# Performance work log

Hardware: AMD Instinct MI355X
Metric: run time of the kernel (lower is better)

## Reference

```python
import jax, jax.numpy as jnp
import numpy as np

D_MODEL = 2048
NUM_HEADS = 16
D_FF = 8192
EPS = 1e-5


def setup_inputs() -> dict:
    key = jax.random.key(0)
    ks = jax.random.split(key, 9)
    s = 0.02
    return {
        "x": jax.random.normal(ks[0], (2, 2048, D_MODEL), dtype=jnp.float32),
        "wq": jax.random.normal(ks[1], (D_MODEL, D_MODEL), dtype=jnp.float32) * s,
        "wk": jax.random.normal(ks[2], (D_MODEL, D_MODEL), dtype=jnp.float32) * s,
        "wv": jax.random.normal(ks[3], (D_MODEL, D_MODEL), dtype=jnp.float32) * s,
        "wo": jax.random.normal(ks[4], (D_MODEL, D_MODEL), dtype=jnp.float32) * s,
        "w1": jax.random.normal(ks[5], (D_FF, D_MODEL), dtype=jnp.float32) * s,
        "w2": jax.random.normal(ks[6], (D_MODEL, D_FF), dtype=jnp.float32) * s,
        "g1": jnp.ones((D_MODEL,), dtype=jnp.float32),
        "g2": jnp.ones((D_MODEL,), dtype=jnp.float32),
    }


def rmsnorm(a, g):
    rms = jnp.sqrt(jnp.sum(a * a, axis=-1, keepdims=True) / a.shape[-1] + EPS)
    return a / rms * g


def attention(xn, wq, wk, wv, wo):
    B, S, D = xn.shape
    H, dk = NUM_HEADS, D // NUM_HEADS
    # Linear weights are (out, in); y = x @ W^T
    q = (xn @ wq.T).reshape(B, S, H, dk).transpose(0, 2, 1, 3)  # bhsd
    k = (xn @ wk.T).reshape(B, S, H, dk).transpose(0, 2, 1, 3)
    v = (xn @ wv.T).reshape(B, S, H, dk).transpose(0, 2, 1, 3)
    scores = jnp.einsum("bhqd,bhkd->bhqk", q, k) * (dk ** -0.5)
    causal = jnp.triu(jnp.ones((S, S), dtype=bool), k=1)
    scores = jnp.where(causal, -jnp.inf, scores)
    probs = jax.nn.softmax(scores, axis=-1)
    out = jnp.einsum("bhqk,bhkd->bhqd", probs, v)
    out = out.transpose(0, 2, 1, 3).reshape(B, S, D)
    return out @ wo.T


def reference(x, wq, wk, wv, wo, w1, w2, g1, g2):
    x = x + attention(rmsnorm(x, g1), wq, wk, wv, wo)
    h = jax.nn.gelu(rmsnorm(x, g2) @ w1.T, approximate=False)
    x = x + h @ w2.T
    return x
```

## Files before the change

### kernel.cpp

```cpp
#include <hip/hip_runtime.h>
#include <hip/hip_bf16.h>
#include <math.h>

#define D_MODEL 2048
#define SEQ     2048
#define BATCH   2
#define NHEAD   16
#define DK      128
#define DFF     8192
#define MROWS   (BATCH*SEQ)

typedef short short8 __attribute__((ext_vector_type(8)));
typedef float f32x4  __attribute__((ext_vector_type(4)));

__device__ __forceinline__ short f2bf(float f) {
  union { __hip_bfloat16 b; short s; } u;
  u.b = __float2bfloat16(f);
  return u.s;
}

__device__ __forceinline__ void gload_lds16(const void* g, void* l) {
  __builtin_amdgcn_global_load_lds(
      (const __attribute__((address_space(1))) unsigned int*)g,
      (__attribute__((address_space(3))) unsigned int*)l, 16, 0, 0);
}

__global__ __launch_bounds__(256) void rmsnorm_k(const float* __restrict__ x,
                                                 const float* __restrict__ g,
                                                 short* __restrict__ o) {
  const int row = blockIdx.x;
  const int t = threadIdx.x;
  const float4* xr = (const float4*)(x + (size_t)row * D_MODEL);
  const float4* gr = (const float4*)g;
  float4 v0 = xr[2*t], v1 = xr[2*t+1];
  float s = v0.x*v0.x + v0.y*v0.y + v0.z*v0.z + v0.w*v0.w
          + v1.x*v1.x + v1.y*v1.y + v1.z*v1.z + v1.w*v1.w;
  #pragma unroll
  for (int off = 1; off < 64; off <<= 1) s += __shfl_xor(s, off);
  __shared__ float red[4];
  if ((t & 63) == 0) red[t >> 6] = s;
  __syncthreads();
  float tot = red[0] + red[1] + red[2] + red[3];
  float inv = rsqrtf(tot * (1.0f / D_MODEL) + 1e-5f);
  float4 g0 = gr[2*t], g1v = gr[2*t+1];
  short8 ov;
  ov[0] = f2bf(v0.x * inv * g0.x);
  ov[1] = f2bf(v0.y * inv * g0.y);
  ov[2] = f2bf(v0.z * inv * g0.z);
  ov[3] = f2bf(v0.w * inv * g0.w);
  ov[4] = f2bf(v1.x * inv * g1v.x);
  ov[5] = f2bf(v1.y * inv * g1v.y);
  ov[6] = f2bf(v1.z * inv * g1v.z);
  ov[7] = f2bf(v1.w * inv * g1v.w);
  *((short8*)(o + (size_t)row * D_MODEL) + t) = ov;
}

__global__ __launch_bounds__(256) void f2b_k(const float* __restrict__ src,
                                             short* __restrict__ dst, int n8) {
  int i = blockIdx.x * 256 + threadIdx.x;
  if (i >= n8) return;
  const float4* s4 = (const float4*)src + 2 * (size_t)i;
  float4 a = s4[0], b = s4[1];
  short8 o = { f2bf(a.x), f2bf(a.y), f2bf(a.z), f2bf(a.w),
               f2bf(b.x), f2bf(b.y), f2bf(b.z), f2bf(b.w) };
  *((short8*)dst + i) = o;
}

template<int EPI>
__global__ __launch_bounds__(256) void gemm_fast(const short* __restrict__ A,
                                                 const short* __restrict__ B,
                                                 void* Cv,
                                                 const float* __restrict__ resid,
                                                 int M, int N, int K) {
  __shared__ __align__(16) short As[128 * 64];
  __shared__ __align__(16) short Bs[128 * 64];
  const int t = threadIdx.x;
  const int m0 = blockIdx.x * 128, n0 = blockIdx.y * 128;
  const int wave = t >> 6, lane = t & 63, lr = lane & 15, lg = lane >> 4;
  const int wr = (wave >> 1) * 64, wc = (wave & 1) * 64;

  f32x4 acc[4][4];
  const f32x4 z4 = {0.f, 0.f, 0.f, 0.f};
  #pragma unroll
  for (int m = 0; m < 4; ++m)
    #pragma unroll
    for (int n = 0; n < 4; ++n) acc[m][n] = z4;

  const int srow = t >> 3;
  const int scol = (t & 7) * 8;

  for (int k0 = 0; k0 < K; k0 += 64) {
    #pragma unroll
    for (int i = 0; i < 4; ++i) {
      int r = srow + 32 * i;
      gload_lds16(A + (size_t)(m0 + r) * K + k0 + scol, &As[r * 64 + scol]);
      gload_lds16(B + (size_t)(n0 + r) * K + k0 + scol, &Bs[r * 64 + scol]);
    }
    __syncthreads();
    #pragma unroll
    for (int kk = 0; kk < 64; kk += 32) {
      short8 af[4], bfr[4];
      #pragma unroll
      for (int m = 0; m < 4; ++m) af[m]  = *(const short8*)&As[(wr + m*16 + lr) * 64 + kk + lg*8];
      #pragma unroll
      for (int n = 0; n < 4; ++n) bfr[n] = *(const short8*)&Bs[(wc + n*16 + lr) * 64 + kk + lg*8];
      #pragma unroll
      for (int m = 0; m < 4; ++m)
        #pragma unroll
        for (int n = 0; n < 4; ++n)
          acc[m][n] = __builtin_amdgcn_mfma_f32_16x16x32_bf16(af[m], bfr[n], acc[m][n], 0, 0, 0);
    }
    __syncthreads();
  }

  #pragma unroll
  for (int m = 0; m < 4; ++m)
    #pragma unroll
    for (int n = 0; n < 4; ++n)
      #pragma unroll
      for (int r = 0; r < 4; ++r) {
        int row = m0 + wr + m*16 + lg*4 + r;
        int col = n0 + wc + n*16 + lr;
        size_t idx = (size_t)row * N + col;
        float vv = acc[m][n][r];
        if (EPI == 0) {
          ((short*)Cv)[idx] = f2bf(vv);
        } else if (EPI == 1) {
          float gl = 0.5f * vv * (1.0f + erff(vv * 0.70710678118654752f));
          ((short*)Cv)[idx] = f2bf(gl);
        } else {
          ((float*)Cv)[idx] = vv + resid[idx];
        }
      }
}

__global__ __launch_bounds__(256) void vtrans(const short* __restrict__ QKV,
                                              short* __restrict__ VT) {
  const int st = blockIdx.x;
  const int bh = blockIdx.y;
  const int b = bh >> 4, h = bh & 15;
  const int t = threadIdx.x;
  __shared__ __align__(16) short T[64 * 128];
  const short* Vsrc = QKV + ((size_t)b * SEQ) * 6144 + 2 * D_MODEL + h * DK;
  {
    int r = t >> 4, c = (t & 15) * 8;
    #pragma unroll
    for (int i = 0; i < 4; ++i) {
      int rr = r + 16 * i;
      uint4 vv = *(const uint4*)(Vsrc + (size_t)(st * 64 + rr) * 6144 + c);
      *(uint4*)&T[rr * 128 + (c ^ (((rr >> 3) & 7) << 3))] = vv;
    }
  }
  __syncthreads();
  short* dst = VT + ((size_t)bh * DK) * SEQ + st * 64;
  {
    int c2 = (t & 7) * 8;
    #pragma unroll
    for (int i = 0; i < 4; ++i) {
      int d = (t >> 3) + 32 * i;
      short8 ov;
      #pragma unroll
      for (int j = 0; j < 8; ++j)
        ov[j] = T[(c2 + j) * 128 + (d ^ ((((c2 + j) >> 3) & 7) << 3))];
      *(short8*)(dst + (size_t)d * SEQ + c2) = ov;
    }
  }
}

__global__ __launch_bounds__(512, 2) void attn3(const short* __restrict__ QKV,
                                                const short* __restrict__ VT,
                                                short* __restrict__ O) {
  const float SC = 0.12751743f;
  const int a = blockIdx.x, bh = blockIdx.y;
  const int b = bh >> 4, h = bh & 15;
  const int t = threadIdx.x, w = t >> 6, lane = t & 63, lr = lane & 15, lg = lane >> 4;
  const short* Qp = QKV + ((size_t)b * SEQ) * 6144 + h * DK;
  const short* Kp = Qp + D_MODEL;
  const short* Vp = VT + ((size_t)bh * DK) * SEQ;
  __shared__ __align__(16) short Ks[2][64 * 128];
  __shared__ __align__(16) short Vs[2][128 * 64];
  __shared__ __align__(16) short Ps[8][16][72];

  const int krr = t >> 4, kcc = (t & 15) * 8;
  const int vdd = t >> 3, vcc = (t & 7) * 8;
  const f32x4 z4 = {0.f, 0.f, 0.f, 0.f};

  for (int sub = 0; sub < 2; ++sub) {
    const int ts = sub ? (15 - a) : a;
    const int nt = 2 * ts + 2;
    const int qrow0 = ts * 128 + w * 16;

    short8 qf[4];
    #pragma unroll
    for (int ki = 0; ki < 4; ++ki)
      qf[ki] = *(const short8*)(Qp + (size_t)(qrow0 + lr) * 6144 + ki * 32 + lg * 8);

    f32x4 acc[8];
    #pragma unroll
    for (int nd = 0; nd < 8; ++nd) acc[nd] = z4;
    float mrow[4], lsum[4];
    #pragma unroll
    for (int r = 0; r < 4; ++r) { mrow[r] = -INFINITY; lsum[r] = 0.f; }

    uint4 krg[2], vrg[2];
    #pragma unroll
    for (int i = 0; i < 2; ++i) {
      krg[i] = *(const uint4*)(Kp + (size_t)(krr + 32 * i) * 6144 + kcc);
      vrg[i] = *(const uint4*)(Vp + (size_t)(vdd + 64 * i) * SEQ + vcc);
    }
    __syncthreads();
    #pragma unroll
    for (int i = 0; i < 2; ++i) {
      int r = krr + 32 * i;
      *(uint4*)&Ks[0][(r * 128 + kcc) ^ ((r & 7) << 3)] = krg[i];
      int d = vdd + 64 * i;
      *(uint4*)&Vs[0][(d * 64 + vcc) ^ ((d & 7) << 3)] = vrg[i];
    }
    __syncthreads();

    int cur = 0;
    for (int tt = 0; tt < nt; ++tt) {
      const bool pre = (tt + 1 < nt);
      if (pre) {
        #pragma unroll
        for (int i = 0; i < 2; ++i) {
          krg[i] = *(const uint4*)(Kp + (size_t)((tt + 1) * 64 + krr + 32 * i) * 6144 + kcc);
          vrg[i] = *(const uint4*)(Vp + (size_t)(vdd + 64 * i) * SEQ + (tt + 1) * 64 + vcc);
        }
      }

      f32x4 sf[4] = {z4, z4, z4, z4};
      #pragma unroll
      for (int ki = 0; ki < 4; ++ki) {
        #pragma unroll
        for (int nk = 0; nk < 4; ++nk) {
          int rr = nk * 16 + lr;
          short8 kf = *(const short8*)&Ks[cur][(rr * 128 + ki * 32 + lg * 8) ^ ((rr & 7) << 3)];
          sf[nk] = __builtin_amdgcn_mfma_f32_16x16x32_bf16(qf[ki], kf, sf[nk], 0, 0, 0);
        }
      }

      const bool diag = (tt * 64 + 63 > qrow0);
      #pragma unroll
      for (int r = 0; r < 4; ++r) {
        int qg = qrow0 + lg * 4 + r;
        float s0 = sf[0][r] * SC, s1 = sf[1][r] * SC, s2 = sf[2][r] * SC, s3 = sf[3][r] * SC;
        if (diag) {
          int c0 = tt * 64 + lr;
          s0 = (c0      <= qg) ? s0 : -3.0e38f;
          s1 = (c0 + 16 <= qg) ? s1 : -3.0e38f;
          s2 = (c0 + 32 <= qg) ? s2 : -3.0e38f;
          s3 = (c0 + 48 <= qg) ? s3 : -3.0e38f;
        }
        float mx = fmaxf(fmaxf(s0, s1), fmaxf(s2, s3));
        mx = fmaxf(mx, __shfl_xor(mx, 1));
        mx = fmaxf(mx, __shfl_xor(mx, 2));
        mx = fmaxf(mx, __shfl_xor(mx, 4));
        mx = fmaxf(mx, __shfl_xor(mx, 8));
        float mnew = fmaxf(mrow[r], mx);
        float alpha = exp2f(mrow[r] - mnew);
        mrow[r] = mnew;
        float p0 = exp2f(s0 - mnew), p1 = exp2f(s1 - mnew),
              p2 = exp2f(s2 - mnew), p3 = exp2f(s3 - mnew);
        lsum[r] = lsum[r] * alpha + ((p0 + p1) + (p2 + p3));
        #pragma unroll
        for (int nd = 0; nd < 8; ++nd) acc[nd][r] *= alpha;
        short* pr = &Ps[w][lg * 4 + r][0];
        pr[lr]      = f2bf(p0);
        pr[16 + lr] = f2bf(p1);
        pr[32 + lr] = f2bf(p2);
        pr[48 + lr] = f2bf(p3);
      }
      asm volatile("s_waitcnt lgkmcnt(0)" ::: "memory");
      __builtin_amdgcn_sched_barrier(0);

      short8 pf0 = *(const short8*)&Ps[w][lr][lg * 8];
      short8 pf1 = *(const short8*)&Ps[w][lr][32 + lg * 8];
      #pragma unroll
      for (int nd = 0; nd < 8; ++nd) {
        int rr = nd * 16 + lr;
        short8 vf0 = *(const short8*)&Vs[cur][(rr * 64 + lg * 8) ^ ((rr & 7) << 3)];
        short8 vf1 = *(const short8*)&Vs[cur][(rr * 64 + 32 + lg * 8) ^ ((rr & 7) << 3)];
        acc[nd] = __builtin_amdgcn_mfma_f32_16x16x32_bf16(pf0, vf0, acc[nd], 0, 0, 0);
        acc[nd] = __builtin_amdgcn_mfma_f32_16x16x32_bf16(pf1, vf1, acc[nd], 0, 0, 0);
      }
      __syncthreads();
      if (pre) {
        #pragma unroll
        for (int i = 0; i < 2; ++i) {
          int r = krr + 32 * i;
          *(uint4*)&Ks[cur ^ 1][(r * 128 + kcc) ^ ((r & 7) << 3)] = krg[i];
          int d = vdd + 64 * i;
          *(uint4*)&Vs[cur ^ 1][(d * 64 + vcc) ^ ((d & 7) << 3)] = vrg[i];
        }
      }
      __syncthreads();
      cur ^= 1;
    }

    float inv[4];
    #pragma unroll
    for (int r = 0; r < 4; ++r) {
      float ls = lsum[r];
      ls += __shfl_xor(ls, 1);
      ls += __shfl_xor(ls, 2);
      ls += __shfl_xor(ls, 4);
      ls += __shfl_xor(ls, 8);
      inv[r] = 1.0f / ls;
    }
    #pragma unroll
    for (int nd = 0; nd < 8; ++nd)
      #pragma unroll
      for (int r = 0; r < 4; ++r) {
        int row = qrow0 + lg * 4 + r;
        O[(size_t)(b * SEQ + row) * D_MODEL + h * DK + nd * 16 + lr] = f2bf(acc[nd][r] * inv[r]);
      }
  }
}

template<int EPI>
__global__ __launch_bounds__(256) void gemm_bt(const short* __restrict__ A,
                                               const float* __restrict__ B,
                                               void* Cv,
                                               const float* resid,
                                               int M, int N, int K) {
  __shared__ __align__(16) short As[128][72];
  __shared__ __align__(16) short Bs[128][72];
  const int t = threadIdx.x;
  const int m0 = blockIdx.x * 128, n0 = blockIdx.y * 128;
  const int wave = t >> 6, lane = t & 63, lr = lane & 15, lg = lane >> 4;
  const int wr = (wave >> 1) * 64, wc = (wave & 1) * 64;

  f32x4 acc[4][4];
  const f32x4 z4 = {0.f, 0.f, 0.f, 0.f};
  #pragma unroll
  for (int m = 0; m < 4; ++m)
    #pragma unroll
    for (int n = 0; n < 4; ++n) acc[m][n] = z4;

  int ar[4], ac[4];
  #pragma unroll
  for (int i = 0; i < 4; ++i) { int u = t + 256*i; ar[i] = u >> 3; ac[i] = (u & 7) * 8; }

  for (int k0 = 0; k0 < K; k0 += 64) {
    #pragma unroll
    for (int i = 0; i < 4; ++i) {
      uint4 va = *(const uint4*)(A + (size_t)(m0 + ar[i]) * K + k0 + ac[i]);
      *(uint4*)&As[ar[i]][ac[i]] = va;
    }
    #pragma unroll
    for (int i = 0; i < 4; ++i) {
      const float4* bp = (const float4*)(B + (size_t)(n0 + ar[i]) * K + k0 + ac[i]);
      float4 b0 = bp[0], b1 = bp[1];
      short8 pb = { f2bf(b0.x), f2bf(b0.y), f2bf(b0.z), f2bf(b0.w),
                    f2bf(b1.x), f2bf(b1.y), f2bf(b1.z), f2bf(b1.w) };
      *(short8*)&Bs[ar[i]][ac[i]] = pb;
    }
    __syncthreads();
    #pragma unroll
    for (int kk = 0; kk < 64; kk += 32) {
      short8 af[4], bfr[4];
      #pragma unroll
      for (int m = 0; m < 4; ++m) af[m]  = *(const short8*)&As[wr + m*16 + lr][kk + lg*8];
      #pragma unroll
      for (int n = 0; n < 4; ++n) bfr[n] = *(const short8*)&Bs[wc + n*16 + lr][kk + lg*8];
      #pragma unroll
      for (int m = 0; m < 4; ++m)
        #pragma unroll
        for (int n = 0; n < 4; ++n)
          acc[m][n] = __builtin_amdgcn_mfma_f32_16x16x32_bf16(af[m], bfr[n], acc[m][n], 0, 0, 0);
    }
    __syncthreads();
  }

  #pragma unroll
  for (int m = 0; m < 4; ++m)
    #pragma unroll
    for (int n = 0; n < 4; ++n)
      #pragma unroll
      for (int r = 0; r < 4; ++r) {
        int row = m0 + wr + m*16 + lg*4 + r;
        int col = n0 + wc + n*16 + lr;
        size_t idx = (size_t)row * N + col;
        float vv = acc[m][n][r];
        if (EPI == 0) {
          ((short*)Cv)[idx] = f2bf(vv);
        } else if (EPI == 1) {
          float gl = 0.5f * vv * (1.0f + erff(vv * 0.70710678118654752f));
          ((short*)Cv)[idx] = f2bf(gl);
        } else {
          ((float*)Cv)[idx] = vv + resid[idx];
        }
      }
}

__global__ __launch_bounds__(256) void attn_k(const short* __restrict__ Q,
                                              const short* __restrict__ K,
                                              const short* __restrict__ V,
                                              short* __restrict__ O) {
  const float scale = 0.08838834764831845f;
  const int qt = blockIdx.x;
  const int bh = blockIdx.y;
  const int b = bh >> 4, h = bh & 15;
  const size_t base = ((size_t)b * SEQ) * D_MODEL + (size_t)h * DK;
  const int t = threadIdx.x, wave = t >> 6, lane = t & 63, lr = lane & 15, lg = lane >> 4;

  __shared__ __align__(16) short Ks[32][136];
  __shared__ __align__(16) short Vt[128][40];
  __shared__ __align__(16) short Ps[4][32][40];

  const int qrow0 = qt * 128 + wave * 32;
  short8 qf[2][4];
  #pragma unroll
  for (int mq = 0; mq < 2; ++mq)
    #pragma unroll
    for (int ki = 0; ki < 4; ++ki)
      qf[mq][ki] = *(const short8*)(Q + base + (size_t)(qrow0 + mq*16 + lr) * D_MODEL + ki*32 + lg*8);

  f32x4 acc[2][8];
  const f32x4 z4 = {0.f, 0.f, 0.f, 0.f};
  #pragma unroll
  for (int mq = 0; mq < 2; ++mq)
    #pragma unroll
    for (int nd = 0; nd < 8; ++nd) acc[mq][nd] = z4;
  float mrow[2][4], lsum[2][4];
  #pragma unroll
  for (int mq = 0; mq < 2; ++mq)
    #pragma unroll
    for (int r = 0; r < 4; ++r) { mrow[mq][r] = -INFINITY; lsum[mq][r] = 0.f; }

  const int lastt = qt * 4 + 3;
  for (int tt = 0; tt <= lastt; ++tt) {
    #pragma unroll
    for (int i = 0; i < 2; ++i) {
      int u = t + 256*i; int r = u >> 4; int c = (u & 15) * 8;
      *(uint4*)&Ks[r][c] = *(const uint4*)(K + base + (size_t)(tt*32 + r) * D_MODEL + c);
      uint4 vv = *(const uint4*)(V + base + (size_t)(tt*32 + r) * D_MODEL + c);
      const short* sv = (const short*)&vv;
      #pragma unroll
      for (int j = 0; j < 8; ++j) Vt[c + j][r] = sv[j];
    }
    __syncthreads();
    if (tt <= qt * 4 + wave) {
      f32x4 sf[2][2] = {{z4, z4}, {z4, z4}};
      #pragma unroll
      for (int ki = 0; ki < 4; ++ki) {
        short8 kf0 = *(const short8*)&Ks[lr][ki*32 + lg*8];
        short8 kf1 = *(const short8*)&Ks[16 + lr][ki*32 + lg*8];
        sf[0][0] = __builtin_amdgcn_mfma_f32_16x16x32_bf16(qf[0][ki], kf0, sf[0][0], 0, 0, 0);
        sf[0][1] = __builtin_amdgcn_mfma_f32_16x16x32_bf16(qf[0][ki], kf1, sf[0][1], 0, 0, 0);
        sf[1][0] = __builtin_amdgcn_mfma_f32_16x16x32_bf16(qf[1][ki], kf0, sf[1][0], 0, 0, 0);
        sf[1][1] = __builtin_amdgcn_mfma_f32_16x16x32_bf16(qf[1][ki], kf1, sf[1][1], 0, 0, 0);
      }
      #pragma unroll
      for (int mq = 0; mq < 2; ++mq) {
        #pragma unroll
        for (int r = 0; r < 4; ++r) {
          int qg = qrow0 + mq*16 + lg*4 + r;
          float s0 = sf[mq][0][r] * scale;
          float s1 = sf[mq][1][r] * scale;
          if (tt*32 + lr > qg)       s0 = -INFINITY;
          if (tt*32 + 16 + lr > qg)  s1 = -INFINITY;
          float mx = fmaxf(s0, s1);
          mx = fmaxf(mx, __shfl_xor(mx, 1));
          mx = fmaxf(mx, __shfl_xor(mx, 2));
          mx = fmaxf(mx, __shfl_xor(mx, 4));
          mx = fmaxf(mx, __shfl_xor(mx, 8));
          float mnew = fmaxf(mrow[mq][r], mx);
          float alpha = __expf(mrow[mq][r] - mnew);
          mrow[mq][r] = mnew;
          float p0 = __expf(s0 - mnew);
          float p1 = __expf(s1 - mnew);
          float ps = p0 + p1;
          ps += __shfl_xor(ps, 1);
          ps += __shfl_xor(ps, 2);
          ps += __shfl_xor(ps, 4);
          ps += __shfl_xor(ps, 8);
          lsum[mq][r] = lsum[mq][r] * alpha + ps;
          #pragma unroll
          for (int nd = 0; nd < 8; ++nd) acc[mq][nd][r] *= alpha;
          Ps[wave][mq*16 + lg*4 + r][lr]      = f2bf(p0);
          Ps[wave][mq*16 + lg*4 + r][16 + lr] = f2bf(p1);
        }
      }
      asm volatile("s_waitcnt lgkmcnt(0)" ::: "memory");
      short8 pf0 = *(const short8*)&Ps[wave][lr][lg*8];
      short8 pf1 = *(const short8*)&Ps[wave][16 + lr][lg*8];
      #pragma unroll
      for (int nd = 0; nd < 8; ++nd) {
        short8 vf = *(const short8*)&Vt[nd*16 + lr][lg*8];
        acc[0][nd] = __builtin_amdgcn_mfma_f32_16x16x32_bf16(pf0, vf, acc[0][nd], 0, 0, 0);
        acc[1][nd] = __builtin_amdgcn_mfma_f32_16x16x32_bf16(pf1, vf, acc[1][nd], 0, 0, 0);
      }
    }
    __syncthreads();
  }

  #pragma unroll
  for (int mq = 0; mq < 2; ++mq)
    #pragma unroll
    for (int nd = 0; nd < 8; ++nd)
      #pragma unroll
      for (int r = 0; r < 4; ++r) {
        int row = qrow0 + mq*16 + lg*4 + r;
        O[base + (size_t)row * D_MODEL + nd*16 + lr] = f2bf(acc[mq][nd][r] / lsum[mq][r]);
      }
}

extern "C" void kernel_launch(void* const* d_in, const int* in_sizes, int n_in,
                              void* d_out, int out_size, void* d_ws, size_t ws_size,
                              hipStream_t stream) {
  const float* x  = (const float*)d_in[0];
  const float* wq = (const float*)d_in[1];
  const float* wk = (const float*)d_in[2];
  const float* wv = (const float*)d_in[3];
  const float* wo = (const float*)d_in[4];
  const float* w1 = (const float*)d_in[5];
  const float* w2 = (const float*)d_in[6];
  const float* g1 = (const float*)d_in[7];
  const float* g2 = (const float*)d_in[8];
  float* out = (float*)d_out;
  char* ws = (char*)d_ws;

  const size_t NEED = (size_t)192 << 20;
  if (ws_size >= NEED) {
    short* wqkv = (short*)(ws);
    short* wo_b = (short*)(ws + ((size_t)24 << 20));
    short* w1_b = (short*)(ws + ((size_t)32 << 20));
    short* w2_b = (short*)(ws + ((size_t)64 << 20));
    short* qkv  = (short*)(ws + ((size_t)96 << 20));
    short* vt   = (short*)(ws + ((size_t)144 << 20));
    short* ab   = (short*)(ws + ((size_t)160 << 20));
    short* xn   = (short*)(ws + ((size_t)176 << 20));
    short* hb   = (short*)(ws + ((size_t)96 << 20));

    const int NW = D_MODEL * D_MODEL / 8;
    f2b_k<<<(NW + 255) / 256, 256, 0, stream>>>(wq, wqkv,                   NW);
    f2b_k<<<(NW + 255) / 256, 256, 0, stream>>>(wk, wqkv + (size_t)D_MODEL * D_MODEL,     NW);
    f2b_k<<<(NW + 255) / 256, 256, 0, stream>>>(wv, wqkv + (size_t)2 * D_MODEL * D_MODEL, NW);
    f2b_k<<<(NW + 255) / 256, 256, 0, stream>>>(wo, wo_b, NW);
    const int NF = DFF * D_MODEL / 8;
    f2b_k<<<(NF + 255) / 256, 256, 0, stream>>>(w1, w1_b, NF);
    f2b_k<<<(NF + 255) / 256, 256, 0, stream>>>(w2, w2_b, NF);

    rmsnorm_k<<<MROWS, 256, 0, stream>>>(x, g1, xn);
    gemm_fast<0><<<dim3(MROWS/128, 6144/128), 256, 0, stream>>>(xn, wqkv, qkv, nullptr, MROWS, 6144, D_MODEL);
    vtrans<<<dim3(SEQ/64, BATCH*NHEAD), 256, 0, stream>>>(qkv, vt);
    attn3<<<dim3(8, BATCH*NHEAD), 512, 0, stream>>>(qkv, vt, ab);
    gemm_fast<2><<<dim3(MROWS/128, D_MODEL/128), 256, 0, stream>>>(ab, wo_b, out, x, MROWS, D_MODEL, D_MODEL);
    rmsnorm_k<<<MROWS, 256, 0, stream>>>(out, g2, xn);
    gemm_fast<1><<<dim3(MROWS/128, DFF/128), 256, 0, stream>>>(xn, w1_b, hb, nullptr, MROWS, DFF, D_MODEL);
    gemm_fast<2><<<dim3(MROWS/128, D_MODEL/128), 256, 0, stream>>>(hb, w2_b, out, out, MROWS, D_MODEL, DFF);
  } else {
    short* qb = (short*)(ws + ((size_t)0  << 20));
    short* kb = (short*)(ws + ((size_t)16 << 20));
    short* vb = (short*)(ws + ((size_t)32 << 20));
    short* ab = (short*)(ws + ((size_t)48 << 20));
    short* xn = (short*)(ws + ((size_t)64 << 20));
    short* hb = (short*)(ws + ((size_t)0  << 20));

    dim3 gproj(MROWS / 128, D_MODEL / 128);
    rmsnorm_k<<<MROWS, 256, 0, stream>>>(x, g1, xn);
    gemm_bt<0><<<gproj, 256, 0, stream>>>(xn, wq, qb, nullptr, MROWS, D_MODEL, D_MODEL);
    gemm_bt<0><<<gproj, 256, 0, stream>>>(xn, wk, kb, nullptr, MROWS, D_MODEL, D_MODEL);
    gemm_bt<0><<<gproj, 256, 0, stream>>>(xn, wv, vb, nullptr, MROWS, D_MODEL, D_MODEL);
    attn_k<<<dim3(SEQ / 128, BATCH * NHEAD), 256, 0, stream>>>(qb, kb, vb, ab);
    gemm_bt<2><<<gproj, 256, 0, stream>>>(ab, wo, out, x, MROWS, D_MODEL, D_MODEL);
    rmsnorm_k<<<MROWS, 256, 0, stream>>>(out, g2, xn);
    for (int half = 0; half < 2; ++half) {
      const short* xh = xn  + (size_t)half * 2048 * D_MODEL;
      float*       oh = out + (size_t)half * 2048 * D_MODEL;
      gemm_bt<1><<<dim3(2048 / 128, DFF / 128), 256, 0, stream>>>(xh, w1, hb, nullptr, 2048, DFF, D_MODEL);
      gemm_bt<2><<<dim3(2048 / 128, D_MODEL / 128), 256, 0, stream>>>(hb, w2, oh, oh, 2048, D_MODEL, DFF);
    }
  }
}
```

Before: 917.1 us.

## Add split-K GEMMs with swizzled LDS, XCD-aware block remap and bf16 combine

Replaces the 2D-grid GEMM with a 1D-grid kernel that remaps block indices across the eight XCDs and XOR-swizzles the LDS layout to avoid bank conflicts. It also sets an occupancy hint of four blocks and drops the trailing barrier on the last iteration. The two N=2048 output projections (Wo and W2) now split K in two and write bf16 partials. A new combine kernel then adds both partials and the residual in fp32. This raises the small-N GEMMs' block count to fill the GPU, at the cost of extra partial-buffer traffic and a bf16 rounding of the partial sums.

```diff
diff --git a/kernel.cpp b/kernel.cpp
--- a/kernel.cpp
+++ b/kernel.cpp
@@ -18,6 +18,13 @@
   u.b = __float2bfloat16(f);
   return u.s;
 }
+__device__ __forceinline__ float bf2f(short s) {
+  union { unsigned u; float f; } u;
+  u.u = ((unsigned)(unsigned short)s) << 16;
+  return u.f;
+}
+
+#define MF(a, b, c) __builtin_amdgcn_mfma_f32_16x16x32_bf16(a, b, c, 0, 0, 0)
 
 __device__ __forceinline__ void gload_lds16(const void* g, void* l) {
   __builtin_amdgcn_global_load_lds(
@@ -66,18 +73,55 @@
   *((short8*)dst + i) = o;
 }
 
-template<int EPI>
-__global__ __launch_bounds__(256) void gemm_fast(const short* __restrict__ A,
-                                                 const short* __restrict__ B,
-                                                 void* Cv,
-                                                 const float* __restrict__ resid,
-                                                 int M, int N, int K) {
+__global__ __launch_bounds__(256) void combine_bb(const short* __restrict__ p0,
+                                                  const short* __restrict__ p1,
+                                                  const float* __restrict__ r,
+                                                  float* __restrict__ o, int n8) {
+  int i = blockIdx.x * 256 + threadIdx.x;
+  if (i >= n8) return;
+  short8 a = ((const short8*)p0)[i];
+  short8 b = ((const short8*)p1)[i];
+  float4 r0 = ((const float4*)r)[2 * (size_t)i];
+  float4 r1 = ((const float4*)r)[2 * (size_t)i + 1];
+  float4 o0, o1;
+  o0.x = bf2f(a[0]) + bf2f(b[0]) + r0.x;
+  o0.y = bf2f(a[1]) + bf2f(b[1]) + r0.y;
+  o0.z = bf2f(a[2]) + bf2f(b[2]) + r0.z;
+  o0.w = bf2f(a[3]) + bf2f(b[3]) + r0.w;
+  o1.x = bf2f(a[4]) + bf2f(b[4]) + r1.x;
+  o1.y = bf2f(a[5]) + bf2f(b[5]) + r1.y;
+  o1.z = bf2f(a[6]) + bf2f(b[6]) + r1.z;
+  o1.w = bf2f(a[7]) + bf2f(b[7]) + r1.w;
+  ((float4*)o)[2 * (size_t)i]     = o0;
+  ((float4*)o)[2 * (size_t)i + 1] = o1;
+}
+
+template<int EPI, int SPLIT>
+__global__ __launch_bounds__(256, 4) void gemm128s(const short* __restrict__ A,
+                                                   const short* __restrict__ Bp,
+                                                   void* Cv,
+                                                   const float* __restrict__ resid,
+                                                   int M, int N, int Kloop,
+                                                   int lda, int nbx) {
   __shared__ __align__(16) short As[128 * 64];
   __shared__ __align__(16) short Bs[128 * 64];
-  const int t = threadIdx.x;
-  const int m0 = blockIdx.x * 128, n0 = blockIdx.y * 128;
-  const int wave = t >> 6, lane = t & 63, lr = lane & 15, lg = lane >> 4;
-  const int wr = (wave >> 1) * 64, wc = (wave & 1) * 64;
+  const int nk = Kloop >> 6;
+  const int cpx = gridDim.x >> 3;
+  const int lin = (blockIdx.x & 7) * cpx + (blockIdx.x >> 3);
+  const int bx = lin % nbx;
+  int row2 = lin / nbx, by, ks = 0;
+  if (SPLIT) { ks = row2 & 1; by = row2 >> 1; } else { by = row2; }
+  const int m0 = bx * 128, n0 = by * 128;
+  if (SPLIT) { A += (size_t)ks * Kloop; Bp += (size_t)ks * Kloop; }
+
+  const int t = threadIdx.x, w = t >> 6, lane = t & 63, lr = lane & 15, lg = lane >> 4;
+  const int wm = w >> 1, wn = w & 1;
+
+  const int r = t >> 3, c8 = t & 7;
+  const int swc = (c8 ^ (r & 7)) << 3;
+  const short* pA = A  + (size_t)(m0 + r) * lda + swc;
+  const short* pB = Bp + (size_t)(n0 + r) * lda + swc;
+  const size_t l32 = (size_t)32 * lda;
 
   f32x4 acc[4][4];
   const f32x4 z4 = {0.f, 0.f, 0.f, 0.f};
@@ -86,45 +130,54 @@
     #pragma unroll
     for (int n = 0; n < 4; ++n) acc[m][n] = z4;
 
-  const int srow = t >> 3;
-  const int scol = (t & 7) * 8;
-
-  for (int k0 = 0; k0 < K; k0 += 64) {
-    #pragma unroll
-    for (int i = 0; i < 4; ++i) {
-      int r = srow + 32 * i;
-      gload_lds16(A + (size_t)(m0 + r) * K + k0 + scol, &As[r * 64 + scol]);
-      gload_lds16(B + (size_t)(n0 + r) * K + k0 + scol, &Bs[r * 64 + scol]);
-    }
+  const int rsw = (lr & 7) << 3;
+
+  for (int T = 0; T < nk; ++T) {
+    #pragma unroll
+    for (int i = 0; i < 4; ++i)
+      gload_lds16(pA + (size_t)T * 64 + i * l32, &As[i * 2048 + w * 512]);
+    #pragma unroll
+    for (int i = 0; i < 4; ++i)
+      gload_lds16(pB + (size_t)T * 64 + i * l32, &Bs[i * 2048 + w * 512]);
     __syncthreads();
-    #pragma unroll
-    for (int kk = 0; kk < 64; kk += 32) {
-      short8 af[4], bfr[4];
-      #pragma unroll
-      for (int m = 0; m < 4; ++m) af[m]  = *(const short8*)&As[(wr + m*16 + lr) * 64 + kk + lg*8];
-      #pragma unroll
-      for (int n = 0; n < 4; ++n) bfr[n] = *(const short8*)&Bs[(wc + n*16 + lr) * 64 + kk + lg*8];
-      #pragma unroll
-      for (int m = 0; m < 4; ++m)
-        #pragma unroll
-        for (int n = 0; n < 4; ++n)
-          acc[m][n] = __builtin_amdgcn_mfma_f32_16x16x32_bf16(af[m], bfr[n], acc[m][n], 0, 0, 0);
-    }
-    __syncthreads();
+
+    short8 af[4][2], bfv[4][2];
+    #pragma unroll
+    for (int m = 0; m < 4; ++m) {
+      int ar = wm * 64 + m * 16 + lr;
+      af[m][0] = *(const short8*)&As[ar * 64 + ((lg * 8) ^ rsw)];
+      af[m][1] = *(const short8*)&As[ar * 64 + ((32 + lg * 8) ^ rsw)];
+    }
+    #pragma unroll
+    for (int n = 0; n < 4; ++n) {
+      int br = wn * 64 + n * 16 + lr;
+      bfv[n][0] = *(const short8*)&Bs[br * 64 + ((lg * 8) ^ rsw)];
+      bfv[n][1] = *(const short8*)&Bs[br * 64 + ((32 + lg * 8) ^ rsw)];
+    }
+    #pragma unroll
+    for (int m = 0; m < 4; ++m)
+      #pragma unroll
+      for (int n = 0; n < 4; ++n) {
+        acc[m][n] = MF(af[m][0], bfv[n][0], acc[m][n]);
+        acc[m][n] = MF(af[m][1], bfv[n][1], acc[m][n]);
+      }
+    if (T + 1 < nk) __syncthreads();
   }
 
+  short* Cs = (short*)Cv;
+  if (SPLIT) Cs += (size_t)ks * ((size_t)M * N);
   #pragma unroll
   for (int m = 0; m < 4; ++m)
     #pragma unroll
     for (int n = 0; n < 4; ++n)
       #pragma unroll
-      for (int r = 0; r < 4; ++r) {
-        int row = m0 + wr + m*16 + lg*4 + r;
-        int col = n0 + wc + n*16 + lr;
+      for (int rr = 0; rr < 4; ++rr) {
+        int row = m0 + wm * 64 + m * 16 + lg * 4 + rr;
+        int col = n0 + wn * 64 + n * 16 + lr;
         size_t idx = (size_t)row * N + col;
-        float vv = acc[m][n][r];
+        float vv = acc[m][n][rr];
         if (EPI == 0) {
-          ((short*)Cv)[idx] = f2bf(vv);
+          Cs[idx] = f2bf(vv);
         } else if (EPI == 1) {
           float gl = 0.5f * vv * (1.0f + erff(vv * 0.70710678118654752f));
           ((short*)Cv)[idx] = f2bf(gl);
@@ -236,7 +289,7 @@
         for (int nk = 0; nk < 4; ++nk) {
           int rr = nk * 16 + lr;
           short8 kf = *(const short8*)&Ks[cur][(rr * 128 + ki * 32 + lg * 8) ^ ((rr & 7) << 3)];
-          sf[nk] = __builtin_amdgcn_mfma_f32_16x16x32_bf16(qf[ki], kf, sf[nk], 0, 0, 0);
+          sf[nk] = MF(qf[ki], kf, sf[nk]);
         }
       }
 
@@ -281,8 +334,8 @@
         int rr = nd * 16 + lr;
         short8 vf0 = *(const short8*)&Vs[cur][(rr * 64 + lg * 8) ^ ((rr & 7) << 3)];
         short8 vf1 = *(const short8*)&Vs[cur][(rr * 64 + 32 + lg * 8) ^ ((rr & 7) << 3)];
-        acc[nd] = __builtin_amdgcn_mfma_f32_16x16x32_bf16(pf0, vf0, acc[nd], 0, 0, 0);
-        acc[nd] = __builtin_amdgcn_mfma_f32_16x16x32_bf16(pf1, vf1, acc[nd], 0, 0, 0);
+        acc[nd] = MF(pf0, vf0, acc[nd]);
+        acc[nd] = MF(pf1, vf1, acc[nd]);
       }
       __syncthreads();
       if (pre) {
@@ -368,7 +421,7 @@
       for (int m = 0; m < 4; ++m)
         #pragma unroll
         for (int n = 0; n < 4; ++n)
-          acc[m][n] = __builtin_amdgcn_mfma_f32_16x16x32_bf16(af[m], bfr[n], acc[m][n], 0, 0, 0);
+          acc[m][n] = MF(af[m], bfr[n], acc[m][n]);
     }
     __syncthreads();
   }
@@ -447,10 +500,10 @@
       for (int ki = 0; ki < 4; ++ki) {
         short8 kf0 = *(const short8*)&Ks[lr][ki*32 + lg*8];
         short8 kf1 = *(const short8*)&Ks[16 + lr][ki*32 + lg*8];
-        sf[0][0] = __builtin_amdgcn_mfma_f32_16x16x32_bf16(qf[0][ki], kf0, sf[0][0], 0, 0, 0);
-        sf[0][1] = __builtin_amdgcn_mfma_f32_16x16x32_bf16(qf[0][ki], kf1, sf[0][1], 0, 0, 0);
-        sf[1][0] = __builtin_amdgcn_mfma_f32_16x16x32_bf16(qf[1][ki], kf0, sf[1][0], 0, 0, 0);
-        sf[1][1] = __builtin_amdgcn_mfma_f32_16x16x32_bf16(qf[1][ki], kf1, sf[1][1], 0, 0, 0);
+        sf[0][0] = MF(qf[0][ki], kf0, sf[0][0]);
+        sf[0][1] = MF(qf[0][ki], kf1, sf[0][1]);
+        sf[1][0] = MF(qf[1][ki], kf0, sf[1][0]);
+        sf[1][1] = MF(qf[1][ki], kf1, sf[1][1]);
       }
       #pragma unroll
       for (int mq = 0; mq < 2; ++mq) {
@@ -489,8 +542,8 @@
       #pragma unroll
       for (int nd = 0; nd < 8; ++nd) {
         short8 vf = *(const short8*)&Vt[nd*16 + lr][lg*8];
-        acc[0][nd] = __builtin_amdgcn_mfma_f32_16x16x32_bf16(pf0, vf, acc[0][nd], 0, 0, 0);
-        acc[1][nd] = __builtin_amdgcn_mfma_f32_16x16x32_bf16(pf1, vf, acc[1][nd], 0, 0, 0);
+        acc[0][nd] = MF(pf0, vf, acc[0][nd]);
+        acc[1][nd] = MF(pf1, vf, acc[1][nd]);
       }
     }
     __syncthreads();
@@ -533,6 +586,8 @@
     short* ab   = (short*)(ws + ((size_t)160 << 20));
     short* xn   = (short*)(ws + ((size_t)176 << 20));
     short* hb   = (short*)(ws + ((size_t)96 << 20));
+    short* po   = (short*)(ws + ((size_t)96 << 20));
+    short* pf   = (short*)(ws + ((size_t)160 << 20));
 
     const int NW = D_MODEL * D_MODEL / 8;
     f2b_k<<<(NW + 255) / 256, 256, 0, stream>>>(wq, wqkv,                   NW);
@@ -543,14 +598,22 @@
     f2b_k<<<(NF + 255) / 256, 256, 0, stream>>>(w1, w1_b, NF);
     f2b_k<<<(NF + 255) / 256, 256, 0, stream>>>(w2, w2_b, NF);
 
+    const int N8 = MROWS * D_MODEL / 8;
+
     rmsnorm_k<<<MROWS, 256, 0, stream>>>(x, g1, xn);
-    gemm_fast<0><<<dim3(MROWS/128, 6144/128), 256, 0, stream>>>(xn, wqkv, qkv, nullptr, MROWS, 6144, D_MODEL);
+    gemm128s<0,0><<<dim3(32 * 48), 256, 0, stream>>>(xn, wqkv, qkv, nullptr,
+                                                     MROWS, 6144, D_MODEL, D_MODEL, 32);
     vtrans<<<dim3(SEQ/64, BATCH*NHEAD), 256, 0, stream>>>(qkv, vt);
     attn3<<<dim3(8, BATCH*NHEAD), 512, 0, stream>>>(qkv, vt, ab);
-    gemm_fast<2><<<dim3(MROWS/128, D_MODEL/128), 256, 0, stream>>>(ab, wo_b, out, x, MROWS, D_MODEL, D_MODEL);
+    gemm128s<0,1><<<dim3(32 * 16 * 2), 256, 0, stream>>>(ab, wo_b, po, nullptr,
+                                                         MROWS, D_MODEL, D_MODEL / 2, D_MODEL, 32);
+    combine_bb<<<(N8 + 255) / 256, 256, 0, stream>>>(po, po + (size_t)MROWS * D_MODEL, x, out, N8);
     rmsnorm_k<<<MROWS, 256, 0, stream>>>(out, g2, xn);
-    gemm_fast<1><<<dim3(MROWS/128, DFF/128), 256, 0, stream>>>(xn, w1_b, hb, nullptr, MROWS, DFF, D_MODEL);
-    gemm_fast<2><<<dim3(MROWS/128, D_MODEL/128), 256, 0, stream>>>(hb, w2_b, out, out, MROWS, D_MODEL, DFF);
+    gemm128s<1,0><<<dim3(32 * 64), 256, 0, stream>>>(xn, w1_b, hb, nullptr,
+                                                     MROWS, DFF, D_MODEL, D_MODEL, 32);
+    gemm128s<0,1><<<dim3(32 * 16 * 2), 256, 0, stream>>>(hb, w2_b, pf, nullptr,
+                                                         MROWS, D_MODEL, DFF / 2, DFF, 32);
+    combine_bb<<<(N8 + 255) / 256, 256, 0, stream>>>(pf, pf + (size_t)MROWS * D_MODEL, out, out, N8);
   } else {
     short* qb = (short*)(ws + ((size_t)0  << 20));
     short* kb = (short*)(ws + ((size_t)16 << 20));
```

After: 757.1 us. 1.21x faster.
